# Performance work log

Measured on AMD Instinct MI355X. Metric: run time of the kernel, lower is better.

Reference implementation:

```python
import jax, jax.numpy as jnp
import numpy as np

N_HEAD = 12
D_HEAD = 64


def setup_inputs() -> dict:
    key = jax.random.key(0)
    ks = jax.random.split(key, 9)
    bs, seq, d_model = 4, 2048, 768
    sc = 1.0 / np.sqrt(d_model)
    return {
        "q": jax.random.normal(ks[0], (bs, seq, d_model), jnp.float32),
        "k": jax.random.normal(ks[1], (bs, seq, d_model), jnp.float32),
        "v": jax.random.normal(ks[2], (bs, seq, d_model), jnp.float32),
        "Wq": jax.random.normal(ks[3], (d_model, d_model), jnp.float32) * sc,
        "bq": jax.random.normal(ks[4], (d_model,), jnp.float32) * 0.01,
        "Wk": jax.random.normal(ks[5], (d_model, d_model), jnp.float32) * sc,
        "bk": jax.random.normal(ks[6], (d_model,), jnp.float32) * 0.01,
        "Wv": jax.random.normal(ks[7], (d_model, d_model), jnp.float32) * sc,
        "bv": jax.random.normal(ks[8], (d_model,), jnp.float32) * 0.01,
    }


def _split_heads(x):
    # [bs, seq, n_head*d_head] -> [bs, n_head, seq, d_head]
    bs, seq, _ = x.shape
    return x.reshape(bs, seq, N_HEAD, D_HEAD).transpose(0, 2, 1, 3)


def reference(q, k, v, Wq, bq, Wk, bk, Wv, bv):
    # Linear projections (torch Linear: x @ W.T + b)
    wq = _split_heads(q @ Wq.T + bq)
    wk = _split_heads(k @ Wk.T + bk)
    wv = _split_heads(v @ Wv.T + bv)
    # scale=False in defaults -> raw dot products, no mask, dropout is eval no-op
    scores = jnp.einsum("bhqd,bhkd->bhqk", wq, wk)  # [bs, h, S, S]
    probs = jax.nn.softmax(scores, axis=-1)
    attn_vec = jnp.einsum("bhqk,bhkd->bhqd", probs, wv)
    bs, _, seq, _ = attn_vec.shape
    # merge heads -> [bs, seq, n_head*d_head]
    return attn_vec.transpose(0, 2, 1, 3).reshape(bs, seq, N_HEAD * D_HEAD)
```

## Files before the change

### kernel.cpp

```cpp
#include <hip/hip_runtime.h>
#include <stdint.h>

typedef _Float16 half8  __attribute__((ext_vector_type(8)));
typedef _Float16 half4v __attribute__((ext_vector_type(4)));
typedef float    floatx4 __attribute__((ext_vector_type(4)));

#define LOG2E 1.44269504088896340736f

__device__ __forceinline__ void gl_lds16(const _Float16* g, _Float16* l) {
  __builtin_amdgcn_global_load_lds(
      (__attribute__((address_space(1))) void*)g,
      (__attribute__((address_space(3))) void*)l, 16, 0, 0);
}

struct CvtArgs {
  const float* src[6];
  _Float16*    dst[6];
  int          n[6];
};

__global__ void cvt_kernel(CvtArgs a) {
  const int z = blockIdx.y;
  const int n = a.n[z];
  const int i = (blockIdx.x * 256 + threadIdx.x) * 8;
  if (i >= n) return;
  const float4* s = (const float4*)(a.src[z] + i);
  float4 v0 = s[0], v1 = s[1];
  half8 h = { (_Float16)v0.x, (_Float16)v0.y, (_Float16)v0.z, (_Float16)v0.w,
              (_Float16)v1.x, (_Float16)v1.y, (_Float16)v1.z, (_Float16)v1.w };
  *(half8*)(a.dst[z] + i) = h;
}

__global__ __launch_bounds__(256, 2) void qkv_gemm(
    const _Float16* __restrict__ xh, const _Float16* __restrict__ wh,
    const float* __restrict__ bqp, const float* __restrict__ bkp, const float* __restrict__ bvp,
    _Float16* __restrict__ oq, _Float16* __restrict__ ok, _Float16* __restrict__ ovt)
{
  __shared__ __attribute__((aligned(16))) _Float16 As[128 * 32];
  __shared__ __attribute__((aligned(16))) _Float16 Bs[128 * 32];
  const int z  = blockIdx.z;
  const _Float16* X = xh + (size_t)z * 8192 * 768;
  const _Float16* W = wh + (size_t)z * 768 * 768;
  const int m0 = blockIdx.x * 128, n0 = blockIdx.y * 128;
  const int tid  = threadIdx.x;
  const int lane = tid & 63, wid = tid >> 6;
  const int wr = wid >> 1, wc = wid & 1;
  const int qd = lane >> 4, col = lane & 15;

  const floatx4 z4 = {0.f, 0.f, 0.f, 0.f};
  floatx4 acc[4][4];
  #pragma unroll
  for (int i = 0; i < 4; ++i)
    #pragma unroll
    for (int j = 0; j < 4; ++j) acc[i][j] = z4;

  const int c0 = tid, c1 = 256 + tid;
  const int ar0 = c0 >> 2, ac0 = (c0 & 3) * 8;
  const int ar1 = c1 >> 2, ac1 = (c1 & 3) * 8;

  for (int k0 = 0; k0 < 768; k0 += 32) {
    __syncthreads();
    gl_lds16(X + (size_t)(m0 + ar0) * 768 + k0 + ac0, As + c0 * 8);
    gl_lds16(X + (size_t)(m0 + ar1) * 768 + k0 + ac1, As + c1 * 8);
    gl_lds16(W + (size_t)(n0 + ar0) * 768 + k0 + ac0, Bs + c0 * 8);
    gl_lds16(W + (size_t)(n0 + ar1) * 768 + k0 + ac1, Bs + c1 * 8);
    __syncthreads();
    half8 af[4], bf[4];
    #pragma unroll
    for (int t = 0; t < 4; ++t)
      af[t] = *(const half8*)(As + (wr * 64 + t * 16 + col) * 32 + qd * 8);
    #pragma unroll
    for (int t = 0; t < 4; ++t)
      bf[t] = *(const half8*)(Bs + (wc * 64 + t * 16 + col) * 32 + qd * 8);
    #pragma unroll
    for (int i = 0; i < 4; ++i)
      #pragma unroll
      for (int j = 0; j < 4; ++j)
        acc[i][j] = __builtin_amdgcn_mfma_f32_16x16x32_f16(af[i], bf[j], acc[i][j], 0, 0, 0);
  }

  const float* bias = (z == 0) ? bqp : ((z == 1) ? bkp : bvp);
  if (z == 2) {
    #pragma unroll
    for (int j = 0; j < 4; ++j) {
      int n = n0 + wc * 64 + j * 16 + col;
      float bb = bias[n];
      #pragma unroll
      for (int i = 0; i < 4; ++i) {
        int m = m0 + wr * 64 + i * 16 + qd * 4;
        int b = m >> 11, s = m & 2047;
        half4v h;
        #pragma unroll
        for (int r = 0; r < 4; ++r) h[r] = (_Float16)(acc[i][j][r] + bb);
        *(half4v*)(ovt + ((size_t)(b * 768 + n)) * 2048 + s) = h;
      }
    }
  } else {
    _Float16* O = (z == 0) ? oq : ok;
    const float scale = (z == 0) ? LOG2E : 1.0f;
    #pragma unroll
    for (int j = 0; j < 4; ++j) {
      int n = n0 + wc * 64 + j * 16 + col;
      float bb = bias[n];
      int hh = n >> 6, d = n & 63;
      #pragma unroll
      for (int i = 0; i < 4; ++i) {
        int m = m0 + wr * 64 + i * 16 + qd * 4;
        int b = m >> 11, s = m & 2047;
        _Float16* p = O + (size_t)(b * 12 + hh) * 131072 + (size_t)s * 64 + d;
        #pragma unroll
        for (int r = 0; r < 4; ++r) p[(size_t)r * 64] = (_Float16)((acc[i][j][r] + bb) * scale);
      }
    }
  }
}


__device__ __forceinline__ void stage_kv(const _Float16* __restrict__ Kg,
                                         const _Float16* __restrict__ Vg,
                                         _Float16* ksd, _Float16* vsd, int j0, int tid) {
  #pragma unroll
  for (int i = 0; i < 2; ++i) {
    int c = i * 256 + tid;
    int row = c >> 3, sc = c & 7;
    gl_lds16(Kg + (size_t)(j0 + row) * 64 + ((sc ^ (row & 7)) * 8), ksd + c * 8);
    gl_lds16(Vg + (size_t)row * 2048 + j0 + ((sc ^ (row & 7)) * 8), vsd + c * 8);
  }
}

template <int BUF>
__device__ __forceinline__ void attn_body(
    int jnext, const _Float16* __restrict__ Kg, const _Float16* __restrict__ Vg,
    _Float16* Ks, _Float16* Vs, int tid,
    const half8 (&qf)[2][2], int kb0, int kb1, const int (&vb)[4],
    float (&m)[2], float (&l)[2], floatx4 (&o)[4][2])
{
  if (jnext < 2048)
    stage_kv(Kg, Vg, Ks + (1 - BUF) * 4096, Vs + (1 - BUF) * 4096, jnext, tid);

  const char* ksb = (const char*)Ks;
  const char* vsb = (const char*)Vs;
  const floatx4 z4 = {0.f, 0.f, 0.f, 0.f};

  floatx4 st[4][2];
  #pragma unroll
  for (int t = 0; t < 4; ++t) {
    half8 kf0 = *(const half8*)(ksb + BUF * 8192 + t * 2048 + kb0);
    half8 kf1 = *(const half8*)(ksb + BUF * 8192 + t * 2048 + kb1);
    #pragma unroll
    for (int qt = 0; qt < 2; ++qt) {
      st[t][qt] = __builtin_amdgcn_mfma_f32_16x16x32_f16(kf0, qf[qt][0], z4, 0, 0, 0);
      st[t][qt] = __builtin_amdgcn_mfma_f32_16x16x32_f16(kf1, qf[qt][1], st[t][qt], 0, 0, 0);
    }
  }

  float mn[2], rs[2];
  half4v pf[4][2];
  #pragma unroll
  for (int qt = 0; qt < 2; ++qt) {
    float mx = fmaxf(
        fmaxf(fmaxf(fmaxf(st[0][qt][0], st[0][qt][1]), fmaxf(st[0][qt][2], st[0][qt][3])),
              fmaxf(fmaxf(st[1][qt][0], st[1][qt][1]), fmaxf(st[1][qt][2], st[1][qt][3]))),
        fmaxf(fmaxf(fmaxf(st[2][qt][0], st[2][qt][1]), fmaxf(st[2][qt][2], st[2][qt][3])),
              fmaxf(fmaxf(st[3][qt][0], st[3][qt][1]), fmaxf(st[3][qt][2], st[3][qt][3]))));
    mx = fmaxf(mx, __shfl_xor(mx, 16, 64));
    mx = fmaxf(mx, __shfl_xor(mx, 32, 64));
    mn[qt] = fmaxf(m[qt], mx);
  }
  bool upd = (mn[0] > m[0]) || (mn[1] > m[1]);

  #pragma unroll
  for (int qt = 0; qt < 2; ++qt) {
    float r = 0.f;
    #pragma unroll
    for (int t = 0; t < 4; ++t) {
      float e0 = __builtin_amdgcn_exp2f(st[t][qt][0] - mn[qt]);
      float e1 = __builtin_amdgcn_exp2f(st[t][qt][1] - mn[qt]);
      float e2 = __builtin_amdgcn_exp2f(st[t][qt][2] - mn[qt]);
      float e3 = __builtin_amdgcn_exp2f(st[t][qt][3] - mn[qt]);
      auto lo = __builtin_amdgcn_cvt_pkrtz(e0, e1);
      auto hi = __builtin_amdgcn_cvt_pkrtz(e2, e3);
      half4v p = {static_cast<_Float16>(lo[0]), static_cast<_Float16>(lo[1]),
                  static_cast<_Float16>(hi[0]), static_cast<_Float16>(hi[1])};
      pf[t][qt] = p;
      r += (e0 + e1) + (e2 + e3);
    }
    r += __shfl_xor(r, 16, 64);
    r += __shfl_xor(r, 32, 64);
    rs[qt] = r;
  }

  if (__any(upd)) {
    #pragma unroll
    for (int qt = 0; qt < 2; ++qt) {
      float alpha = __builtin_amdgcn_exp2f(m[qt] - mn[qt]);
      m[qt] = mn[qt];
      l[qt] = l[qt] * alpha + rs[qt];
      #pragma unroll
      for (int dt = 0; dt < 4; ++dt) {
        o[dt][qt][0] *= alpha; o[dt][qt][1] *= alpha;
        o[dt][qt][2] *= alpha; o[dt][qt][3] *= alpha;
      }
    }
  } else {
    l[0] += rs[0];
    l[1] += rs[1];
  }

  #pragma unroll
  for (int dt = 0; dt < 4; ++dt) {
    #pragma unroll
    for (int t = 0; t < 4; ++t) {
      half4v vf = *(const half4v*)(vsb + BUF * 8192 + dt * 2048 + vb[t]);
      #pragma unroll
      for (int qt = 0; qt < 2; ++qt)
        o[dt][qt] = __builtin_amdgcn_mfma_f32_16x16x16f16(vf, pf[t][qt], o[dt][qt], 0, 0, 0);
    }
  }
  __syncthreads();
}

__global__ __launch_bounds__(256, 3) void attn_kernel(
    const _Float16* __restrict__ Qm,
    const _Float16* __restrict__ Km,
    const _Float16* __restrict__ Vt,
    float* __restrict__ out)
{
  __shared__ __attribute__((aligned(16))) _Float16 Ks[2 * 4096];
  __shared__ __attribute__((aligned(16))) _Float16 Vs[2 * 4096];
  const int bh = blockIdx.y;
  const int q0 = blockIdx.x * 128;
  const int tid = threadIdx.x, lane = tid & 63, w = tid >> 6;
  const int qd = lane >> 4, col = lane & 15, c7 = col & 7;
  const _Float16* Qg = Qm + (size_t)bh * 131072;
  const _Float16* Kg = Km + (size_t)bh * 131072;
  const _Float16* Vg = Vt + (size_t)bh * 131072;

  half8 qf[2][2];
  #pragma unroll
  for (int qt = 0; qt < 2; ++qt)
    #pragma unroll
    for (int ks = 0; ks < 2; ++ks)
      qf[qt][ks] = *(const half8*)(Qg + (size_t)(q0 + w * 32 + qt * 16 + col) * 64
                                   + (ks * 4 + qd) * 8);

  const int kb0 = col * 128 + ((qd ^ c7) * 16);
  const int kb1 = col * 128 + (((4 + qd) ^ c7) * 16);
  const int vq = (qd >> 1) ^ c7;
  int vb[4];
  #pragma unroll
  for (int t = 0; t < 4; ++t)
    vb[t] = col * 128 + (qd & 1) * 8 + ((vq ^ (2 * t)) * 16);

  float m[2] = {-1e30f, -1e30f};
  float l[2] = {0.f, 0.f};
  const floatx4 z4 = {0.f, 0.f, 0.f, 0.f};
  floatx4 o[4][2];
  #pragma unroll
  for (int dt = 0; dt < 4; ++dt)
    #pragma unroll
    for (int qt = 0; qt < 2; ++qt) o[dt][qt] = z4;

  stage_kv(Kg, Vg, Ks, Vs, 0, tid);
  __syncthreads();

  for (int jj = 0; jj < 2048; jj += 128) {
    attn_body<0>(jj + 64,  Kg, Vg, Ks, Vs, tid, qf, kb0, kb1, vb, m, l, o);
    attn_body<1>(jj + 128, Kg, Vg, Ks, Vs, tid, qf, kb0, kb1, vb, m, l, o);
  }

  const int b = bh / 12, h = bh % 12;
  #pragma unroll
  for (int qt = 0; qt < 2; ++qt) {
    float inv = 1.0f / l[qt];
    int qg = q0 + w * 32 + qt * 16 + col;
    float* obase = out + ((size_t)b * 2048 + qg) * 768 + h * 64;
    #pragma unroll
    for (int dt = 0; dt < 4; ++dt) {
      floatx4 v = o[dt][qt];
      v[0] *= inv; v[1] *= inv; v[2] *= inv; v[3] *= inv;
      *(floatx4*)(obase + dt * 16 + qd * 4) = v;
    }
  }
}

extern "C" void kernel_launch(void* const* d_in, const int* in_sizes, int n_in,
                              void* d_out, int out_size, void* d_ws, size_t ws_size,
                              hipStream_t stream) {
  const float* q  = (const float*)d_in[0];
  const float* k  = (const float*)d_in[1];
  const float* v  = (const float*)d_in[2];
  const float* Wq = (const float*)d_in[3];
  const float* bq = (const float*)d_in[4];
  const float* Wk = (const float*)d_in[5];
  const float* bk = (const float*)d_in[6];
  const float* Wv = (const float*)d_in[7];
  const float* bv = (const float*)d_in[8];

  const size_t NX = 6291456;
  const size_t NW = 589824;
  const size_t need = (3 * NX + 3 * NW + 3 * NX) * sizeof(_Float16);
  if (ws_size < need) return;

  _Float16* xh = (_Float16*)d_ws;
  _Float16* wh = xh + 3 * NX;
  _Float16* qh = wh + 3 * NW;
  _Float16* kh = qh + NX;
  _Float16* vt = kh + NX;

  CvtArgs ca;
  ca.src[0] = q;  ca.src[1] = k;  ca.src[2] = v;
  ca.src[3] = Wq; ca.src[4] = Wk; ca.src[5] = Wv;
  ca.dst[0] = xh;          ca.dst[1] = xh + NX;     ca.dst[2] = xh + 2 * NX;
  ca.dst[3] = wh;          ca.dst[4] = wh + NW;     ca.dst[5] = wh + 2 * NW;
  ca.n[0] = (int)NX; ca.n[1] = (int)NX; ca.n[2] = (int)NX;
  ca.n[3] = (int)NW; ca.n[4] = (int)NW; ca.n[5] = (int)NW;

  cvt_kernel<<<dim3(3072, 6), 256, 0, stream>>>(ca);
  qkv_gemm<<<dim3(64, 6, 3), 256, 0, stream>>>(xh, wh, bq, bk, bv, qh, kh, vt);
  attn_kernel<<<dim3(16, 48), 256, 0, stream>>>(qh, kh, vt, (float*)d_out);
}
```

Measured before the change: 255.7 us.

## Fold running-max subtraction into MFMA accumulator and compute row sums via MFMA

```diff
diff --git a/kernel.cpp b/kernel.cpp
--- a/kernel.cpp
+++ b/kernel.cpp
@@ -11,6 +11,13 @@
   __builtin_amdgcn_global_load_lds(
       (__attribute__((address_space(1))) void*)g,
       (__attribute__((address_space(3))) void*)l, 16, 0, 0);
+}
+
+__device__ __forceinline__ half4v pack4(float a, float b, float c, float d) {
+  auto lo = __builtin_amdgcn_cvt_pkrtz(a, b);
+  auto hi = __builtin_amdgcn_cvt_pkrtz(c, d);
+  return half4v{static_cast<_Float16>(lo[0]), static_cast<_Float16>(lo[1]),
+                static_cast<_Float16>(hi[0]), static_cast<_Float16>(hi[1])};
 }
 
 struct CvtArgs {
@@ -133,14 +140,13 @@
     int jnext, const _Float16* __restrict__ Kg, const _Float16* __restrict__ Vg,
     _Float16* Ks, _Float16* Vs, int tid,
     const half8 (&qf)[2][2], int kb0, int kb1, const int (&vb)[4],
-    float (&m)[2], float (&l)[2], floatx4 (&o)[4][2])
+    float (&m)[2], floatx4 (&negm)[2], floatx4 (&ol)[2], floatx4 (&o)[4][2])
 {
   if (jnext < 2048)
     stage_kv(Kg, Vg, Ks + (1 - BUF) * 4096, Vs + (1 - BUF) * 4096, jnext, tid);
 
   const char* ksb = (const char*)Ks;
   const char* vsb = (const char*)Vs;
-  const floatx4 z4 = {0.f, 0.f, 0.f, 0.f};
 
   floatx4 st[4][2];
   #pragma unroll
@@ -149,64 +155,56 @@
     half8 kf1 = *(const half8*)(ksb + BUF * 8192 + t * 2048 + kb1);
     #pragma unroll
     for (int qt = 0; qt < 2; ++qt) {
-      st[t][qt] = __builtin_amdgcn_mfma_f32_16x16x32_f16(kf0, qf[qt][0], z4, 0, 0, 0);
+      st[t][qt] = __builtin_amdgcn_mfma_f32_16x16x32_f16(kf0, qf[qt][0], negm[qt], 0, 0, 0);
       st[t][qt] = __builtin_amdgcn_mfma_f32_16x16x32_f16(kf1, qf[qt][1], st[t][qt], 0, 0, 0);
     }
   }
 
-  float mn[2], rs[2];
-  half4v pf[4][2];
+  float mx[2];
   #pragma unroll
   for (int qt = 0; qt < 2; ++qt) {
-    float mx = fmaxf(
+    float v = fmaxf(
         fmaxf(fmaxf(fmaxf(st[0][qt][0], st[0][qt][1]), fmaxf(st[0][qt][2], st[0][qt][3])),
               fmaxf(fmaxf(st[1][qt][0], st[1][qt][1]), fmaxf(st[1][qt][2], st[1][qt][3]))),
         fmaxf(fmaxf(fmaxf(st[2][qt][0], st[2][qt][1]), fmaxf(st[2][qt][2], st[2][qt][3])),
               fmaxf(fmaxf(st[3][qt][0], st[3][qt][1]), fmaxf(st[3][qt][2], st[3][qt][3]))));
-    mx = fmaxf(mx, __shfl_xor(mx, 16, 64));
-    mx = fmaxf(mx, __shfl_xor(mx, 32, 64));
-    mn[qt] = fmaxf(m[qt], mx);
-  }
-  bool upd = (mn[0] > m[0]) || (mn[1] > m[1]);
-
-  #pragma unroll
-  for (int qt = 0; qt < 2; ++qt) {
-    float r = 0.f;
-    #pragma unroll
-    for (int t = 0; t < 4; ++t) {
-      float e0 = __builtin_amdgcn_exp2f(st[t][qt][0] - mn[qt]);
-      float e1 = __builtin_amdgcn_exp2f(st[t][qt][1] - mn[qt]);
-      float e2 = __builtin_amdgcn_exp2f(st[t][qt][2] - mn[qt]);
-      float e3 = __builtin_amdgcn_exp2f(st[t][qt][3] - mn[qt]);
-      auto lo = __builtin_amdgcn_cvt_pkrtz(e0, e1);
-      auto hi = __builtin_amdgcn_cvt_pkrtz(e2, e3);
-      half4v p = {static_cast<_Float16>(lo[0]), static_cast<_Float16>(lo[1]),
-                  static_cast<_Float16>(hi[0]), static_cast<_Float16>(hi[1])};
-      pf[t][qt] = p;
-      r += (e0 + e1) + (e2 + e3);
-    }
-    r += __shfl_xor(r, 16, 64);
-    r += __shfl_xor(r, 32, 64);
-    rs[qt] = r;
-  }
-
+    v = fmaxf(v, __shfl_xor(v, 16, 64));
+    mx[qt] = fmaxf(v, __shfl_xor(v, 32, 64));
+  }
+  bool upd = (mx[0] > 0.f) || (mx[1] > 0.f);
+
+  half4v pf[4][2];
   if (__any(upd)) {
     #pragma unroll
     for (int qt = 0; qt < 2; ++qt) {
-      float alpha = __builtin_amdgcn_exp2f(m[qt] - mn[qt]);
-      m[qt] = mn[qt];
-      l[qt] = l[qt] * alpha + rs[qt];
-      #pragma unroll
-      for (int dt = 0; dt < 4; ++dt) {
-        o[dt][qt][0] *= alpha; o[dt][qt][1] *= alpha;
-        o[dt][qt][2] *= alpha; o[dt][qt][3] *= alpha;
+      float mr = fmaxf(mx[qt], 0.f);
+      float al = __builtin_amdgcn_exp2f(-mr);
+      m[qt] += mr;
+      negm[qt] -= mr;
+      ol[qt] *= al;
+      #pragma unroll
+      for (int dt = 0; dt < 4; ++dt) o[dt][qt] *= al;
+      #pragma unroll
+      for (int t = 0; t < 4; ++t) {
+        pf[t][qt] = pack4(__builtin_amdgcn_exp2f(st[t][qt][0] - mr),
+                          __builtin_amdgcn_exp2f(st[t][qt][1] - mr),
+                          __builtin_amdgcn_exp2f(st[t][qt][2] - mr),
+                          __builtin_amdgcn_exp2f(st[t][qt][3] - mr));
       }
     }
   } else {
-    l[0] += rs[0];
-    l[1] += rs[1];
-  }
-
+    #pragma unroll
+    for (int qt = 0; qt < 2; ++qt)
+      #pragma unroll
+      for (int t = 0; t < 4; ++t) {
+        pf[t][qt] = pack4(__builtin_amdgcn_exp2f(st[t][qt][0]),
+                          __builtin_amdgcn_exp2f(st[t][qt][1]),
+                          __builtin_amdgcn_exp2f(st[t][qt][2]),
+                          __builtin_amdgcn_exp2f(st[t][qt][3]));
+      }
+  }
+
+  const half4v vone = {(_Float16)1.0f, (_Float16)1.0f, (_Float16)1.0f, (_Float16)1.0f};
   #pragma unroll
   for (int dt = 0; dt < 4; ++dt) {
     #pragma unroll
@@ -217,6 +215,12 @@
         o[dt][qt] = __builtin_amdgcn_mfma_f32_16x16x16f16(vf, pf[t][qt], o[dt][qt], 0, 0, 0);
     }
   }
+  #pragma unroll
+  for (int t = 0; t < 4; ++t)
+    #pragma unroll
+    for (int qt = 0; qt < 2; ++qt)
+      ol[qt] = __builtin_amdgcn_mfma_f32_16x16x16f16(vone, pf[t][qt], ol[qt], 0, 0, 0);
+
   __syncthreads();
 }
 
@@ -252,9 +256,10 @@
   for (int t = 0; t < 4; ++t)
     vb[t] = col * 128 + (qd & 1) * 8 + ((vq ^ (2 * t)) * 16);
 
-  float m[2] = {-1e30f, -1e30f};
-  float l[2] = {0.f, 0.f};
+  float m[2] = {-100.f, -100.f};
+  floatx4 negm[2] = {{100.f, 100.f, 100.f, 100.f}, {100.f, 100.f, 100.f, 100.f}};
   const floatx4 z4 = {0.f, 0.f, 0.f, 0.f};
+  floatx4 ol[2] = {z4, z4};
   floatx4 o[4][2];
   #pragma unroll
   for (int dt = 0; dt < 4; ++dt)
@@ -265,20 +270,20 @@
   __syncthreads();
 
   for (int jj = 0; jj < 2048; jj += 128) {
-    attn_body<0>(jj + 64,  Kg, Vg, Ks, Vs, tid, qf, kb0, kb1, vb, m, l, o);
-    attn_body<1>(jj + 128, Kg, Vg, Ks, Vs, tid, qf, kb0, kb1, vb, m, l, o);
+    attn_body<0>(jj + 64,  Kg, Vg, Ks, Vs, tid, qf, kb0, kb1, vb, m, negm, ol, o);
+    attn_body<1>(jj + 128, Kg, Vg, Ks, Vs, tid, qf, kb0, kb1, vb, m, negm, ol, o);
   }
 
   const int b = bh / 12, h = bh % 12;
   #pragma unroll
   for (int qt = 0; qt < 2; ++qt) {
-    float inv = 1.0f / l[qt];
+    float inv = 1.0f / ol[qt][0];
     int qg = q0 + w * 32 + qt * 16 + col;
     float* obase = out + ((size_t)b * 2048 + qg) * 768 + h * 64;
     #pragma unroll
     for (int dt = 0; dt < 4; ++dt) {
       floatx4 v = o[dt][qt];
-      v[0] *= inv; v[1] *= inv; v[2] *= inv; v[3] *= inv;
+      v *= inv;
       *(floatx4*)(obase + dt * 16 + qd * 4) = v;
     }
   }
```

After: 323.6 us. +26.6%, slower.
